# Kernel tuning notes

Hardware: AMD Instinct MI355X
Metric: run time of the kernel (lower is better)

The kernel has to match this reference:

```python
import jax, jax.numpy as jnp
import numpy as np

N = 50000
E = 800000
IN_DIM = 128
HID = 64
HEADS = 4
OUT_DIM = 128


def setup_inputs() -> dict:
    key = jax.random.key(0)
    ks = jax.random.split(key, 12)
    s = lambda fan: 1.0 / np.sqrt(fan)
    return {
        'features': jax.random.normal(ks[0], (N, IN_DIM), jnp.float32),
        'edge_index': jax.random.randint(ks[1], (2, E), 0, N, jnp.int64),
        # layer 1: in_dim -> heads*hid, concat=True
        'W1': jax.random.normal(ks[2], (IN_DIM, HEADS * HID), jnp.float32) * s(IN_DIM),
        'att_src1': jax.random.normal(ks[3], (HEADS, HID), jnp.float32) * s(HID),
        'att_dst1': jax.random.normal(ks[4], (HEADS, HID), jnp.float32) * s(HID),
        'bias1': jnp.zeros((HEADS * HID,), jnp.float32),
        # layer 2: heads*hid -> out_dim, 1 head, concat=False
        'W2': jax.random.normal(ks[5], (HEADS * HID, OUT_DIM), jnp.float32) * s(HEADS * HID),
        'att_src2': jax.random.normal(ks[6], (1, OUT_DIM), jnp.float32) * s(OUT_DIM),
        'att_dst2': jax.random.normal(ks[7], (1, OUT_DIM), jnp.float32) * s(OUT_DIM),
        'bias2': jnp.zeros((OUT_DIM,), jnp.float32),
    }


def _gat_conv(x, src, dst, W, a_src, a_dst, bias, heads, out_ch):
    n = x.shape[0]
    h = (x @ W).reshape(n, heads, out_ch)              # [N, H, C]
    alpha_s = jnp.einsum('nhc,hc->nh', h, a_src)       # [N, H]
    alpha_d = jnp.einsum('nhc,hc->nh', h, a_dst)
    e = jax.nn.leaky_relu(alpha_s[src] + alpha_d[dst], 0.2)  # [E, H]
    # segment softmax over incoming edges of each dst node
    m = jax.ops.segment_max(e, dst, num_segments=n)
    m = jnp.where(jnp.isfinite(m), m, 0.0)
    ex = jnp.exp(e - m[dst])
    denom = jax.ops.segment_sum(ex, dst, num_segments=n)
    alpha = ex / denom[dst]                            # [E, H]
    out = jax.ops.segment_sum(alpha[:, :, None] * h[src], dst, num_segments=n)  # [N, H, C]
    return out.reshape(n, heads * out_ch) + bias


def reference(features, edge_index, W1, att_src1, att_dst1, bias1, W2, att_src2, att_dst2, bias2):
    n = features.shape[0]
    loops = jnp.arange(n, dtype=edge_index.dtype)
    src = jnp.concatenate([edge_index[0], loops])
    dst = jnp.concatenate([edge_index[1], loops])

    act = lambda v: jax.nn.leaky_relu(v, 0.2)
    x = _gat_conv(features, src, dst, W1, att_src1, att_dst1, bias1, HEADS, HID)
    x = act(x)  # dropout inactive (eval)
    x = _gat_conv(x, src, dst, W2, att_src2, att_dst2, bias2, 1, OUT_DIM)
    x = act(x)
    # in_dim == out_dim -> identity residual
    return x + features
```

## Files before the change

kernel.cpp:

```cpp
#include <hip/hip_runtime.h>
#include <math.h>

#define LRELU(x) ((x) > 0.0f ? (x) : 0.2f * (x))

typedef __attribute__((ext_vector_type(8))) short bf16x8;
typedef __attribute__((ext_vector_type(4))) float floatx4;

__device__ __forceinline__ float bf2f(ushort u) {
    union { unsigned u; float f; } v; v.u = ((unsigned)u) << 16; return v.f;
}
__device__ __forceinline__ ushort f2bf(float f) {
    union { float f; unsigned u; } v; v.f = f;
    unsigned r = (v.u + 0x7FFFu + ((v.u >> 16) & 1u)) >> 16;
    return (ushort)r;
}

__global__ __launch_bounds__(256) void prep_kernel(
    const float* __restrict__ feat, const float* __restrict__ W1,
    const float* __restrict__ as1, const float* __restrict__ ad1,
    const float* __restrict__ W2, const float* __restrict__ as2,
    const float* __restrict__ ad2, const int* __restrict__ ei,
    ushort* __restrict__ featb, ushort* __restrict__ Bp1, ushort* __restrict__ Bp2,
    int* __restrict__ deg, ushort* __restrict__ col,
    int N, int E, int Npart, int b_cvt, int b_p1, int b_p2)
{
    const int b = blockIdx.x, t = threadIdx.x;
    if (b < b_cvt) {
        int i = b * 256 + t;
        if (i < N * 32) {
            float4 v = ((const float4*)feat)[i];
            ushort4 o;
            o.x = f2bf(v.x); o.y = f2bf(v.y); o.z = f2bf(v.z); o.w = f2bf(v.w);
            ((ushort4*)featb)[i] = o;
        }
    } else if (b < b_cvt + b_p1) {
        int i = (b - b_cvt) * 256 + t;
        if (i < 272 * 128) {
            int n = i / 128, k = i % 128;
            float v;
            if (n < 256) v = W1[k * 256 + n];
            else if (n < 260) {
                int h = n - 256; float s = 0.f;
                for (int c = 0; c < 64; ++c) s += W1[k * 256 + h * 64 + c] * as1[h * 64 + c];
                v = s;
            } else if (n < 264) {
                int h = n - 260; float s = 0.f;
                for (int c = 0; c < 64; ++c) s += W1[k * 256 + h * 64 + c] * ad1[h * 64 + c];
                v = s;
            } else v = 0.f;
            Bp1[i] = f2bf(v);
        }
    } else if (b < b_cvt + b_p1 + b_p2) {
        int i = (b - b_cvt - b_p1) * 256 + t;
        if (i < 144 * 256) {
            int n = i / 256, k = i % 256;
            float v;
            if (n < 128) v = W2[k * 128 + n];
            else if (n == 128) {
                float s = 0.f;
                for (int c = 0; c < 128; ++c) s += W2[k * 128 + c] * as2[c];
                v = s;
            } else if (n == 129) {
                float s = 0.f;
                for (int c = 0; c < 128; ++c) s += W2[k * 128 + c] * ad2[c];
                v = s;
            } else v = 0.f;
            Bp2[i] = f2bf(v);
        }
    } else {
        const int fb = b - b_cvt - b_p1 - b_p2;
        const int part = fb & 7;
        const int base = (fb >> 3) * 8192;
        const int lo = part * Npart;
        const int hi = min(N, lo + Npart);
        for (int q0 = 0; q0 < 32; q0 += 4) {
            int dsts[4]; bool val[4];
#pragma unroll
            for (int u = 0; u < 4; ++u) {
                int k = base + (q0 + u) * 256 + t;
                val[u] = k < E;
                if (val[u]) dsts[u] = ei[E + k];
            }
#pragma unroll
            for (int u = 0; u < 4; ++u) {
                if (val[u] && dsts[u] >= lo && dsts[u] < hi) {
                    int k = base + (q0 + u) * 256 + t;
                    int src = ei[k];
                    int slot = atomicAdd(&deg[dsts[u]], 1);
                    if (slot < 63) col[dsts[u] * 64 + slot] = (ushort)src;
                }
            }
        }
    }
}

__global__ __launch_bounds__(256) void gemm_attn1_kernel(
    const ushort* __restrict__ A, const ushort* __restrict__ Bp,
    float* __restrict__ as_, float* __restrict__ ad_, int M)
{
    const int lane = threadIdx.x & 63;
    const int wave = threadIdx.x >> 6;
    const int quad = lane >> 4;
    const int l16  = lane & 15;
    const int row0 = blockIdx.x * 64 + wave * 16;
    const int arow = min(row0 + l16, M - 1);
    const ushort* ap = A + (size_t)arow * 128 + quad * 8;
    const ushort* bp = Bp + (size_t)(256 + l16) * 128 + quad * 8;

    floatx4 acc = (floatx4){0.f, 0.f, 0.f, 0.f};
#pragma unroll
    for (int k0 = 0; k0 < 128; k0 += 32) {
        bf16x8 a = *(const bf16x8*)(ap + k0);
        bf16x8 b = *(const bf16x8*)(bp + k0);
        acc = __builtin_amdgcn_mfma_f32_16x16x32_bf16(a, b, acc, 0, 0, 0);
    }
#pragma unroll
    for (int r = 0; r < 4; ++r) {
        int row = row0 + quad * 4 + r;
        if (row < M) {
            float v = acc[r];
            if (l16 < 4)      as_[row * 4 + l16] = v;
            else if (l16 < 8) ad_[row * 4 + (l16 - 4)] = v;
        }
    }
}

__global__ __launch_bounds__(256) void gat_gather1_kernel(
    const int* __restrict__ deg, const ushort* __restrict__ col,
    const float* __restrict__ as_, const float* __restrict__ ad_,
    const ushort* __restrict__ xb, ushort* __restrict__ aggx, int N)
{
    __shared__ float4 alph[4][64];
    const int lane = threadIdx.x & 63;
    const int wave = threadIdx.x >> 6;
    const int n = blockIdx.x * 4 + wave;
    if (n >= N) return;
    const int dgE = min(deg[n], 63);
    const float4 ad4 = *(const float4*)(ad_ + n * 4);

    int src = n;
    float4 ex4 = {0.f, 0.f, 0.f, 0.f};
    if (lane <= dgE) {
        if (lane < dgE) src = col[n * 64 + lane];
        float4 a4 = *(const float4*)(as_ + src * 4);
        ex4.x = __expf(LRELU(a4.x + ad4.x));
        ex4.y = __expf(LRELU(a4.y + ad4.y));
        ex4.z = __expf(LRELU(a4.z + ad4.z));
        ex4.w = __expf(LRELU(a4.w + ad4.w));
        alph[wave][lane] = ex4;
    }
    float sx = ex4.x, sy = ex4.y, sz = ex4.z, sw = ex4.w;
#pragma unroll
    for (int m = 1; m < 64; m <<= 1) {
        sx += __shfl_xor(sx, m, 64); sy += __shfl_xor(sy, m, 64);
        sz += __shfl_xor(sz, m, 64); sw += __shfl_xor(sw, m, 64);
    }
    const float rd[4] = {1.0f / sx, 1.0f / sy, 1.0f / sz, 1.0f / sw};

    const int esl = lane >> 5;
    const int ch0 = (lane & 31) * 4;
    const int dg = dgE + 1;
    float acc[4][4] = {};
    for (int j0 = 0; j0 < dg; j0 += 8) {
        ushort4 u[4]; float4 a[4]; bool v[4]; int jj[4];
#pragma unroll
        for (int q = 0; q < 4; ++q) {
            jj[q] = j0 + 2 * q + esl;
            v[q] = jj[q] < dg;
            if (v[q]) {
                int s = __shfl(src, jj[q], 64);
                a[q] = alph[wave][jj[q]];
                u[q] = *(const ushort4*)(xb + (size_t)s * 128 + ch0);
            }
        }
#pragma unroll
        for (int q = 0; q < 4; ++q) {
            if (v[q]) {
                float f0 = bf2f(u[q].x), f1 = bf2f(u[q].y), f2 = bf2f(u[q].z), f3 = bf2f(u[q].w);
                acc[0][0] += a[q].x * f0; acc[0][1] += a[q].x * f1; acc[0][2] += a[q].x * f2; acc[0][3] += a[q].x * f3;
                acc[1][0] += a[q].y * f0; acc[1][1] += a[q].y * f1; acc[1][2] += a[q].y * f2; acc[1][3] += a[q].y * f3;
                acc[2][0] += a[q].z * f0; acc[2][1] += a[q].z * f1; acc[2][2] += a[q].z * f2; acc[2][3] += a[q].z * f3;
                acc[3][0] += a[q].w * f0; acc[3][1] += a[q].w * f1; acc[3][2] += a[q].w * f2; acc[3][3] += a[q].w * f3;
            }
        }
    }
#pragma unroll
    for (int h = 0; h < 4; ++h)
#pragma unroll
        for (int c = 0; c < 4; ++c) acc[h][c] += __shfl_xor(acc[h][c], 32, 64);

    if (lane < 32) {
#pragma unroll
        for (int h = 0; h < 4; ++h) {
            ushort4 o;
            o.x = f2bf(acc[h][0] * rd[h]); o.y = f2bf(acc[h][1] * rd[h]);
            o.z = f2bf(acc[h][2] * rd[h]); o.w = f2bf(acc[h][3] * rd[h]);
            *(ushort4*)(aggx + ((size_t)h * N + n) * 128 + ch0) = o;
        }
    }
}

__global__ __launch_bounds__(256) void gemm_l1l2_kernel(
    const ushort* __restrict__ aggx, const ushort* __restrict__ Bp1,
    const float* __restrict__ bias1, const ushort* __restrict__ Bp2,
    ushort* __restrict__ h2b, float* __restrict__ as2_, float* __restrict__ ad2_, int M)
{
    __shared__ ushort x1s[64][264];
    const int lane = threadIdx.x & 63;
    const int wave = threadIdx.x >> 6;
    const int quad = lane >> 4;
    const int l16  = lane & 15;
    const int row0 = blockIdx.x * 64 + wave * 16;
    const int arow = min(row0 + l16, M - 1);

#pragma unroll
    for (int h = 0; h < 4; ++h) {
        const ushort* ap = aggx + ((size_t)h * M + arow) * 128 + quad * 8;
        floatx4 acc[4];
#pragma unroll
        for (int i = 0; i < 4; ++i) acc[i] = (floatx4){0.f, 0.f, 0.f, 0.f};
#pragma unroll
        for (int k0 = 0; k0 < 128; k0 += 32) {
            bf16x8 a = *(const bf16x8*)(ap + k0);
#pragma unroll
            for (int nt = 0; nt < 4; ++nt) {
                bf16x8 b = *(const bf16x8*)(Bp1 + (size_t)(h * 64 + nt * 16 + l16) * 128 + k0 + quad * 8);
                acc[nt] = __builtin_amdgcn_mfma_f32_16x16x32_bf16(a, b, acc[nt], 0, 0, 0);
            }
        }
#pragma unroll
        for (int nt = 0; nt < 4; ++nt) {
            const int c = h * 64 + nt * 16 + l16;
            const float bv = bias1[c];
#pragma unroll
            for (int r = 0; r < 4; ++r)
                x1s[wave * 16 + quad * 4 + r][c] = f2bf(LRELU(acc[nt][r] + bv));
        }
    }
    __syncthreads();

    floatx4 acc2[9];
#pragma unroll
    for (int i = 0; i < 9; ++i) acc2[i] = (floatx4){0.f, 0.f, 0.f, 0.f};
#pragma unroll
    for (int k0 = 0; k0 < 256; k0 += 32) {
        bf16x8 a = *(const bf16x8*)&x1s[wave * 16 + l16][k0 + quad * 8];
#pragma unroll
        for (int nt = 0; nt < 9; ++nt) {
            bf16x8 b = *(const bf16x8*)(Bp2 + (size_t)(nt * 16 + l16) * 256 + k0 + quad * 8);
            acc2[nt] = __builtin_amdgcn_mfma_f32_16x16x32_bf16(a, b, acc2[nt], 0, 0, 0);
        }
    }
#pragma unroll
    for (int nt = 0; nt < 8; ++nt) {
#pragma unroll
        for (int r = 0; r < 4; ++r) {
            int row = row0 + quad * 4 + r;
            if (row < M) h2b[(size_t)row * 128 + nt * 16 + l16] = f2bf(acc2[nt][r]);
        }
    }
#pragma unroll
    for (int r = 0; r < 4; ++r) {
        int row = row0 + quad * 4 + r;
        if (row < M) {
            float v = acc2[8][r];
            if (l16 == 0)      as2_[row] = v;
            else if (l16 == 1) ad2_[row] = v;
        }
    }
}

__global__ __launch_bounds__(256) void gat_gather2_kernel(
    const int* __restrict__ deg, const ushort* __restrict__ col,
    const float* __restrict__ as_, const float* __restrict__ ad_,
    const ushort* __restrict__ h2, const float* __restrict__ bias,
    const float* __restrict__ resid, float* __restrict__ out, int N)
{
    __shared__ float alph[4][64];
    const int lane = threadIdx.x & 63;
    const int wave = threadIdx.x >> 6;
    const int n = blockIdx.x * 4 + wave;
    if (n >= N) return;
    const int dgE = min(deg[n], 63);
    const float adv = ad_[n];

    int src = n;
    float ex = 0.f;
    if (lane <= dgE) {
        if (lane < dgE) src = col[n * 64 + lane];
        ex = __expf(LRELU(as_[src] + adv));
        alph[wave][lane] = ex;
    }
    float s = ex;
#pragma unroll
    for (int m = 1; m < 64; m <<= 1) s += __shfl_xor(s, m, 64);
    const float rden = 1.0f / s;

    const int esl = lane >> 5;
    const int ch0 = (lane & 31) * 4;
    const int dg = dgE + 1;
    float ax = 0.f, ay = 0.f, az = 0.f, aw = 0.f;
    for (int j0 = 0; j0 < dg; j0 += 8) {
        ushort4 u[4]; float a[4]; bool v[4]; int jj[4];
#pragma unroll
        for (int q = 0; q < 4; ++q) {
            jj[q] = j0 + 2 * q + esl;
            v[q] = jj[q] < dg;
            if (v[q]) {
                int sA = __shfl(src, jj[q], 64);
                a[q] = alph[wave][jj[q]];
                u[q] = *(const ushort4*)(h2 + (size_t)sA * 128 + ch0);
            }
        }
#pragma unroll
        for (int q = 0; q < 4; ++q) {
            if (v[q]) {
                ax += a[q] * bf2f(u[q].x); ay += a[q] * bf2f(u[q].y);
                az += a[q] * bf2f(u[q].z); aw += a[q] * bf2f(u[q].w);
            }
        }
    }
    ax += __shfl_xor(ax, 32, 64); ay += __shfl_xor(ay, 32, 64);
    az += __shfl_xor(az, 32, 64); aw += __shfl_xor(aw, 32, 64);

    if (lane < 32) {
        const float4 bv = *(const float4*)(bias + ch0);
        const float4 fv = *(const float4*)(resid + (size_t)n * 128 + ch0);
        float4 o;
        o.x = LRELU(ax * rden + bv.x) + fv.x;
        o.y = LRELU(ay * rden + bv.y) + fv.y;
        o.z = LRELU(az * rden + bv.z) + fv.z;
        o.w = LRELU(aw * rden + bv.w) + fv.w;
        *(float4*)(out + (size_t)n * 128 + ch0) = o;
    }
}

extern "C" void kernel_launch(void* const* d_in, const int* in_sizes, int n_in,
                              void* d_out, int out_size, void* d_ws, size_t ws_size,
                              hipStream_t stream)
{
    const float* feat = (const float*)d_in[0];
    const int*   ei   = (const int*)d_in[1];
    const float* W1   = (const float*)d_in[2];
    const float* asrc1 = (const float*)d_in[3];
    const float* adst1 = (const float*)d_in[4];
    const float* bias1 = (const float*)d_in[5];
    const float* W2    = (const float*)d_in[6];
    const float* asrc2 = (const float*)d_in[7];
    const float* adst2 = (const float*)d_in[8];
    const float* bias2 = (const float*)d_in[9];
    float* outp = (float*)d_out;

    const int IN_DIM = 128, C2 = 128;
    const int N = in_sizes[0] / IN_DIM;
    const int E = in_sizes[1] / 2;

    char* w = (char*)d_ws;
    ushort* featb = (ushort*)w; w += (size_t)N * IN_DIM * 2;
    ushort* aggx  = (ushort*)w; w += (size_t)4 * N * IN_DIM * 2;
    ushort* h2b   = (ushort*)w; w += (size_t)N * C2 * 2;
    ushort* Bp1   = (ushort*)w; w += (size_t)272 * 128 * 2;
    ushort* Bp2   = (ushort*)w; w += (size_t)144 * 256 * 2;
    float* as1_   = (float*)w;  w += (size_t)N * 4 * 4;
    float* ad1_   = (float*)w;  w += (size_t)N * 4 * 4;
    float* as2_   = (float*)w;  w += (size_t)N * 4;
    float* ad2_   = (float*)w;  w += (size_t)N * 4;
    int* deg      = (int*)w;    w += (size_t)N * 4;
    ushort* col   = (ushort*)w; w += (size_t)N * 64 * 2;

    dim3 blk(256);
    const int mg = (N + 63) / 64;
    const int gg = (N + 3) / 4;
    const int Npart = (N + 7) / 8;

    const int b_cvt = (N * 32 + 255) / 256;
    const int b_p1  = (272 * 128 + 255) / 256;
    const int b_p2  = (144 * 256 + 255) / 256;
    const int b_fil = 8 * ((E + 8191) / 8192);

    hipMemsetAsync(deg, 0, (size_t)N * 4, stream);
    prep_kernel<<<dim3(b_cvt + b_p1 + b_p2 + b_fil), blk, 0, stream>>>(
        feat, W1, asrc1, adst1, W2, asrc2, adst2, ei,
        featb, Bp1, Bp2, deg, col, N, E, Npart, b_cvt, b_p1, b_p2);

    gemm_attn1_kernel<<<dim3(mg), blk, 0, stream>>>(featb, Bp1, as1_, ad1_, N);
    gat_gather1_kernel<<<dim3(gg), blk, 0, stream>>>(deg, col, as1_, ad1_, featb, aggx, N);

    gemm_l1l2_kernel<<<dim3(mg), blk, 0, stream>>>(aggx, Bp1, bias1, Bp2, h2b, as2_, ad2_, N);

    gat_gather2_kernel<<<dim3(gg), blk, 0, stream>>>(deg, col, as2_, ad2_, h2b, bias2, feat, outp, N);
}
```

Before: 304.2 us.

## Repartition fused GEMM waves by output columns to reuse B fragments in registers

The fused layer-1/layer-2 GEMM kernel now splits work across waves by output column tile instead of by row tile. Each wave loads its B (weight) fragments once into registers and reuses them across all 64 rows of the block, where before every wave reloaded all weight fragments from global memory. The goal is less redundant weight traffic and more MFMA issue per load. The trade-off is higher register pressure, and in layer 2 wave 3 takes an extra ninth column tile (the attention projections), so the waves are unevenly loaded.

Result: faster. 262.0 us (-13.9%).

```diff
diff --git a/kernel.cpp b/kernel.cpp
--- a/kernel.cpp
+++ b/kernel.cpp
@@ -200,6 +200,50 @@
     }
 }
 
+__device__ __forceinline__ void l2_tile(int ct, const ushort x1s[64][264],
+    const ushort* __restrict__ Bp2, int brow, int M, int lane,
+    ushort* __restrict__ h2b, float* __restrict__ as2_, float* __restrict__ ad2_)
+{
+    const int quad = lane >> 4;
+    const int l16  = lane & 15;
+    bf16x8 bfr[8];
+#pragma unroll
+    for (int kq = 0; kq < 8; ++kq)
+        bfr[kq] = *(const bf16x8*)(Bp2 + (size_t)(ct * 16 + l16) * 256 + kq * 32 + quad * 8);
+
+    floatx4 acc[4];
+#pragma unroll
+    for (int rg = 0; rg < 4; ++rg) acc[rg] = (floatx4){0.f, 0.f, 0.f, 0.f};
+#pragma unroll
+    for (int kq = 0; kq < 8; ++kq) {
+#pragma unroll
+        for (int rg = 0; rg < 4; ++rg) {
+            bf16x8 a = *(const bf16x8*)&x1s[rg * 16 + l16][kq * 32 + quad * 8];
+            acc[rg] = __builtin_amdgcn_mfma_f32_16x16x32_bf16(a, bfr[kq], acc[rg], 0, 0, 0);
+        }
+    }
+    if (ct < 8) {
+#pragma unroll
+        for (int rg = 0; rg < 4; ++rg)
+#pragma unroll
+            for (int r = 0; r < 4; ++r) {
+                int row = brow + rg * 16 + quad * 4 + r;
+                if (row < M) h2b[(size_t)row * 128 + ct * 16 + l16] = f2bf(acc[rg][r]);
+            }
+    } else {
+#pragma unroll
+        for (int rg = 0; rg < 4; ++rg)
+#pragma unroll
+            for (int r = 0; r < 4; ++r) {
+                int row = brow + rg * 16 + quad * 4 + r;
+                if (row < M) {
+                    if (l16 == 0)      as2_[row] = acc[rg][r];
+                    else if (l16 == 1) ad2_[row] = acc[rg][r];
+                }
+            }
+    }
+}
+
 __global__ __launch_bounds__(256) void gemm_l1l2_kernel(
     const ushort* __restrict__ aggx, const ushort* __restrict__ Bp1,
     const float* __restrict__ bias1, const ushort* __restrict__ Bp2,
@@ -210,64 +254,50 @@
     const int wave = threadIdx.x >> 6;
     const int quad = lane >> 4;
     const int l16  = lane & 15;
-    const int row0 = blockIdx.x * 64 + wave * 16;
-    const int arow = min(row0 + l16, M - 1);
-
-#pragma unroll
-    for (int h = 0; h < 4; ++h) {
-        const ushort* ap = aggx + ((size_t)h * M + arow) * 128 + quad * 8;
+    const int brow = blockIdx.x * 64;
+
+    bf16x8 bfr[4][4];
+#pragma unroll
+    for (int nt = 0; nt < 4; ++nt)
+#pragma unroll
+        for (int kq = 0; kq < 4; ++kq)
+            bfr[nt][kq] = *(const bf16x8*)(Bp1 + (size_t)(wave * 64 + nt * 16 + l16) * 128 + kq * 32 + quad * 8);
+
+    bf16x8 afr[4][4];
+#pragma unroll
+    for (int rt = 0; rt < 4; ++rt) {
+        const int arow = min(brow + rt * 16 + l16, M - 1);
+        const ushort* ap = aggx + ((size_t)wave * M + arow) * 128 + quad * 8;
+#pragma unroll
+        for (int kq = 0; kq < 4; ++kq)
+            afr[rt][kq] = *(const bf16x8*)(ap + kq * 32);
+    }
+
+#pragma unroll
+    for (int rt = 0; rt < 4; ++rt) {
         floatx4 acc[4];
 #pragma unroll
-        for (int i = 0; i < 4; ++i) acc[i] = (floatx4){0.f, 0.f, 0.f, 0.f};
-#pragma unroll
-        for (int k0 = 0; k0 < 128; k0 += 32) {
-            bf16x8 a = *(const bf16x8*)(ap + k0);
-#pragma unroll
-            for (int nt = 0; nt < 4; ++nt) {
-                bf16x8 b = *(const bf16x8*)(Bp1 + (size_t)(h * 64 + nt * 16 + l16) * 128 + k0 + quad * 8);
-                acc[nt] = __builtin_amdgcn_mfma_f32_16x16x32_bf16(a, b, acc[nt], 0, 0, 0);
-            }
-        }
+        for (int nt = 0; nt < 4; ++nt) acc[nt] = (floatx4){0.f, 0.f, 0.f, 0.f};
+#pragma unroll
+        for (int kq = 0; kq < 4; ++kq)
+#pragma unroll
+            for (int nt = 0; nt < 4; ++nt)
+                acc[nt] = __builtin_amdgcn_mfma_f32_16x16x32_bf16(afr[rt][kq], bfr[nt][kq], acc[nt], 0, 0, 0);
 #pragma unroll
         for (int nt = 0; nt < 4; ++nt) {
-            const int c = h * 64 + nt * 16 + l16;
+            const int c = wave * 64 + nt * 16 + l16;
             const float bv = bias1[c];
 #pragma unroll
             for (int r = 0; r < 4; ++r)
-                x1s[wave * 16 + quad * 4 + r][c] = f2bf(LRELU(acc[nt][r] + bv));
+                x1s[rt * 16 + quad * 4 + r][c] = f2bf(LRELU(acc[nt][r] + bv));
         }
     }
     __syncthreads();
 
-    floatx4 acc2[9];
-#pragma unroll
-    for (int i = 0; i < 9; ++i) acc2[i] = (floatx4){0.f, 0.f, 0.f, 0.f};
-#pragma unroll
-    for (int k0 = 0; k0 < 256; k0 += 32) {
-        bf16x8 a = *(const bf16x8*)&x1s[wave * 16 + l16][k0 + quad * 8];
-#pragma unroll
-        for (int nt = 0; nt < 9; ++nt) {
-            bf16x8 b = *(const bf16x8*)(Bp2 + (size_t)(nt * 16 + l16) * 256 + k0 + quad * 8);
-            acc2[nt] = __builtin_amdgcn_mfma_f32_16x16x32_bf16(a, b, acc2[nt], 0, 0, 0);
-        }
-    }
-#pragma unroll
-    for (int nt = 0; nt < 8; ++nt) {
-#pragma unroll
-        for (int r = 0; r < 4; ++r) {
-            int row = row0 + quad * 4 + r;
-            if (row < M) h2b[(size_t)row * 128 + nt * 16 + l16] = f2bf(acc2[nt][r]);
-        }
-    }
-#pragma unroll
-    for (int r = 0; r < 4; ++r) {
-        int row = row0 + quad * 4 + r;
-        if (row < M) {
-            float v = acc2[8][r];
-            if (l16 == 0)      as2_[row] = v;
-            else if (l16 == 1) ad2_[row] = v;
-        }
-    }
+    l2_tile(wave * 2,     x1s, Bp2, brow, M, lane, h2b, as2_, ad2_);
+    l2_tile(wave * 2 + 1, x1s, Bp2, brow, M, lane, h2b, as2_, ad2_);
+    if (wave == 3)
+        l2_tile(8,        x1s, Bp2, brow, M, lane, h2b, as2_, ad2_);
 }
 
 __global__ __launch_bounds__(256) void gat_gather2_kernel(
```
